# Kernel optimization log

Measured on AMD Instinct MI355X. Metric: run time of the kernel, lower is better.

Reference implementation:

```python
import jax, jax.numpy as jnp
import numpy as np

D_MODEL = 512
D_INNER = 1024           # expand=2 * d_model
HEADDIM = 1024           # headdim = 2*hidden_dim -> nheads = 1
NHEADS = 1
D_STATE = 128            # Mamba2 default
D_CONV = 4               # Mamba2 default
CONV_DIM = D_INNER + 2 * D_STATE   # 1280
D_IN_PROJ = 2 * D_INNER + 2 * D_STATE + NHEADS  # 2305
BATCH, SEQ = 8, 2048
EPS = 1e-5


def setup_inputs() -> dict:
    key = jax.random.key(0)
    ks = jax.random.split(key, 8)
    x = jax.random.normal(ks[0], (BATCH, SEQ, D_MODEL), dtype=jnp.float32)
    rnn_state = jnp.zeros((1, BATCH, D_MODEL), dtype=jnp.float32)
    W_in = jax.random.normal(ks[1], (D_MODEL, D_IN_PROJ), dtype=jnp.float32) * 0.02
    conv_w = jax.random.normal(ks[2], (CONV_DIM, D_CONV), dtype=jnp.float32) * 0.2
    conv_b = jnp.zeros((CONV_DIM,), dtype=jnp.float32)
    dt_bias = jax.random.normal(ks[3], (NHEADS,), dtype=jnp.float32) * 0.1
    # A in (-16, -1): A_log = log(uniform(1,16))
    A_log = jnp.log(jax.random.uniform(ks[4], (NHEADS,), minval=1.0, maxval=16.0, dtype=jnp.float32))
    D = jnp.ones((NHEADS,), dtype=jnp.float32)
    norm_w = jnp.ones((D_INNER,), dtype=jnp.float32)
    W_out = jax.random.normal(ks[5], (D_INNER, D_MODEL), dtype=jnp.float32) * 0.02
    return {"x": x, "rnn_state": rnn_state, "W_in": W_in, "conv_w": conv_w,
            "conv_b": conv_b, "dt_bias": dt_bias, "A_log": A_log, "D": D,
            "norm_w": norm_w, "W_out": W_out}


def _mamba2_forward(x, W_in, conv_w, conv_b, dt_bias, A_log, D, norm_w, W_out):
    Bsz, T, _ = x.shape
    zxbcdt = x @ W_in                              # [B,T,2305]
    z = zxbcdt[..., :D_INNER]                      # [B,T,1024]
    xBC = zxbcdt[..., D_INNER:D_INNER + CONV_DIM]  # [B,T,1280]
    dt = zxbcdt[..., -NHEADS:]                     # [B,T,1]

    # causal depthwise conv1d over time, then silu
    xBC_t = jnp.transpose(xBC, (0, 2, 1))          # [B,C,T]
    w = conv_w[:, None, :]                          # [C,1,K]
    conv = jax.lax.conv_general_dilated(
        xBC_t, w, window_strides=(1,), padding=[(D_CONV - 1, 0)],
        feature_group_count=CONV_DIM, dimension_numbers=("NCH", "OIH", "NCH"))
    xBC = jax.nn.silu(jnp.transpose(conv, (0, 2, 1)) + conv_b)  # [B,T,1280]

    x_ssm = xBC[..., :D_INNER].reshape(Bsz, T, NHEADS, HEADDIM)  # [B,T,H,P]
    Bm = xBC[..., D_INNER:D_INNER + D_STATE]       # [B,T,N] (ngroups=1)
    Cm = xBC[..., -D_STATE:]                       # [B,T,N]

    dt = jax.nn.softplus(dt + dt_bias)             # [B,T,H]
    A = -jnp.exp(A_log)                            # [H]

    # selective SSM recurrence over time (time-major scan)
    xs = (jnp.transpose(x_ssm, (1, 0, 2, 3)),      # [T,B,H,P]
          jnp.transpose(dt, (1, 0, 2)),            # [T,B,H]
          jnp.transpose(Bm, (1, 0, 2)),            # [T,B,N]
          jnp.transpose(Cm, (1, 0, 2)))            # [T,B,N]
    h0 = jnp.zeros((Bsz, NHEADS, HEADDIM, D_STATE), dtype=x.dtype)

    def step(h, inp):
        xt, dtt, Bt, Ct = inp
        dA = jnp.exp(dtt * A)                      # [B,H]
        h = h * dA[:, :, None, None] + (dtt[:, :, None] * xt)[..., None] * Bt[:, None, None, :]
        y = jnp.einsum("bhpn,bn->bhp", h, Ct)
        return h, y

    _, ys = jax.lax.scan(step, h0, xs)             # ys: [T,B,H,P]
    y = jnp.transpose(ys, (1, 0, 2, 3)) + x_ssm * D[None, None, :, None]
    y = y.reshape(Bsz, T, D_INNER)

    # gated RMSNorm (norm_before_gate=False): rmsnorm(y * silu(z)) * weight
    y = y * jax.nn.silu(z)
    y = y * jax.lax.rsqrt(jnp.mean(y * y, axis=-1, keepdims=True) + EPS) * norm_w
    return y @ W_out                               # [B,T,D_MODEL]


def reference(x, rnn_state, W_in, conv_w, conv_b, dt_bias, A_log, D, norm_w, W_out):
    out = _mamba2_forward(x, W_in, conv_w, conv_b, dt_bias, A_log, D, norm_w, W_out)
    return (out, rnn_state)
```

## Files before the change

kernel.cpp:

```cpp
#include <hip/hip_runtime.h>
#include <hip/hip_bf16.h>
#include <math.h>

#define D_MODEL 512
#define D_INNER 1024
#define D_STATE 128
#define CONV_DIM (D_INNER + 2*D_STATE)
#define D_IN_PROJ (2*D_INNER + 2*D_STATE + 1)
#define NPROJ 2304
#define BATCH 8
#define SEQ 2048
#define NROWS (BATCH*SEQ)
#define CHUNK 128
#define NCHUNK (NROWS/CHUNK)
#define CPB (SEQ/CHUNK)
#define EPS_RMS 1e-5f

typedef __hip_bfloat16 bf16;
typedef __attribute__((ext_vector_type(8))) short short8;
typedef __attribute__((ext_vector_type(4))) float f32x4;

__device__ __forceinline__ float fbf(bf16 v) { return __bfloat162float(v); }
__device__ __forceinline__ bf16 tbf(float v) { return __float2bfloat16(v); }

__device__ __forceinline__ void gl2lds16(const bf16* g, bf16* l) {
    __builtin_amdgcn_global_load_lds(
        (const __attribute__((address_space(1))) unsigned int*)g,
        (__attribute__((address_space(3))) unsigned int*)l, 16, 0, 0);
}


__global__ void k_transpose_cvt(const float* __restrict__ src, bf16* __restrict__ dst,
                                int R, int C, int sstride) {
    __shared__ float tile[32][33];
    int c0 = blockIdx.x * 32, r0 = blockIdx.y * 32;
    int tx = threadIdx.x, ty = threadIdx.y;
    #pragma unroll
    for (int i = 0; i < 32; i += 8)
        tile[ty + i][tx] = src[(size_t)(c0 + ty + i) * sstride + (r0 + tx)];
    __syncthreads();
    #pragma unroll
    for (int i = 0; i < 32; i += 8)
        dst[(size_t)(r0 + ty + i) * C + (c0 + tx)] = tbf(tile[tx][ty + i]);
}

__global__ __launch_bounds__(256) void k_dtcvt(
    const float* __restrict__ x, const float* __restrict__ W_in,
    const float* __restrict__ dt_bias,
    bf16* __restrict__ xb, float* __restrict__ dts)
{
    __shared__ float wcol[D_MODEL];
    int tid = threadIdx.x;
    wcol[tid]       = W_in[(size_t)tid * D_IN_PROJ + 2304];
    wcol[tid + 256] = W_in[(size_t)(tid + 256) * D_IN_PROJ + 2304];
    __syncthreads();
    int row  = blockIdx.x * 4 + (tid >> 6);
    int lane = tid & 63;
    const float* xr = x + (size_t)row * D_MODEL;
    float4 a = *(const float4*)(xr + lane * 8);
    float4 b = *(const float4*)(xr + lane * 8 + 4);
    union { bf16 o[8]; uint4 u; } pk;
    pk.o[0]=tbf(a.x); pk.o[1]=tbf(a.y); pk.o[2]=tbf(a.z); pk.o[3]=tbf(a.w);
    pk.o[4]=tbf(b.x); pk.o[5]=tbf(b.y); pk.o[6]=tbf(b.z); pk.o[7]=tbf(b.w);
    *(uint4*)(xb + (size_t)row * D_MODEL + lane * 8) = pk.u;
    const float* wc = wcol + lane * 8;
    float s = a.x*wc[0]+a.y*wc[1]+a.z*wc[2]+a.w*wc[3]
            + b.x*wc[4]+b.y*wc[5]+b.z*wc[6]+b.w*wc[7];
    #pragma unroll
    for (int off = 32; off; off >>= 1) s += __shfl_xor(s, off);
    if (lane == 0) {
        float raw = s + dt_bias[0];
        dts[row] = raw > 20.f ? raw : log1pf(expf(raw));
    }
}

template<int MODE>
__global__ __launch_bounds__(256) void k_bgemm(
    const bf16* __restrict__ A, int lda, size_t sA,
    const bf16* __restrict__ Bt, int ldb, size_t sB,
    void* __restrict__ Cv, int ldc, size_t sC, int K,
    const float* __restrict__ svec, const float* __restrict__ dts,
    const float* __restrict__ Dp)
{
    constexpr int BK = 64;
    __shared__ __align__(16) bf16 As[128][BK];
    __shared__ __align__(16) bf16 Bs[128][BK];
    const int tid = threadIdx.x, lane = tid & 63, wave = tid >> 6;
    const int wm = (wave & 1) * 64, wn = (wave >> 1) * 64;
    const int lr = lane & 15, quad = lane >> 4;
    const int rx = lr & 7;
    const size_t bm = (size_t)blockIdx.x * 128;
    const size_t bn = (size_t)blockIdx.y * 128;
    const size_t bi = blockIdx.z;
    A  += bi * sA;
    Bt += bi * sB;
    const int srow = lane >> 3;
    const int scol = (((lane & 7) ^ srow) << 3);

    f32x4 acc[4][4];
    #pragma unroll
    for (int i = 0; i < 4; ++i)
        #pragma unroll
        for (int j = 0; j < 4; ++j) acc[i][j] = (f32x4){0.f,0.f,0.f,0.f};

    for (int k0 = 0; k0 < K; k0 += BK) {
        __syncthreads();
        #pragma unroll
        for (int q = 0; q < 4; ++q) {
            int rg = wave * 32 + q * 8;
            gl2lds16(A  + (bm + rg + srow) * lda + k0 + scol, &As[rg][0]);
            gl2lds16(Bt + (bn + rg + srow) * ldb + k0 + scol, &Bs[rg][0]);
        }
        __syncthreads();
        #pragma unroll
        for (int ks = 0; ks < BK; ks += 32) {
            const int off = ((((ks >> 3) + quad) ^ rx) << 3);
            short8 af[4], bg[4];
            #pragma unroll
            for (int i = 0; i < 4; ++i)
                af[i] = *(const short8*)(&As[wm + i*16 + lr][off]);
            #pragma unroll
            for (int j = 0; j < 4; ++j)
                bg[j] = *(const short8*)(&Bs[wn + j*16 + lr][off]);
            #pragma unroll
            for (int i = 0; i < 4; ++i)
                #pragma unroll
                for (int j = 0; j < 4; ++j)
                    acc[i][j] = __builtin_amdgcn_mfma_f32_16x16x32_bf16(af[i], bg[j], acc[i][j], 0,0,0);
        }
    }
    const int rb = (int)bi * CHUNK;
    #pragma unroll
    for (int i = 0; i < 4; ++i)
        #pragma unroll
        for (int j = 0; j < 4; ++j)
            #pragma unroll
            for (int r = 0; r < 4; ++r) {
                size_t row = bm + wm + i*16 + quad*4 + r;
                size_t col = bn + wn + j*16 + lr;
                float v = acc[i][j][r];
                if (MODE == 0) {
                    ((float*)Cv + bi*sC)[row * ldc + col] = v;
                } else if (MODE == 1) {
                    ((bf16*)Cv + bi*sC)[row * ldc + col] = tbf(v);
                } else {
                    float o = 0.f;
                    if (col <= row) {
                        o = v * expf(svec[rb + row] - svec[rb + col]) * dts[rb + col];
                        if (col == row) o += Dp[0];
                    }
                    ((bf16*)Cv + bi*sC)[row * ldc + col] = tbf(o);
                }
            }
}

__global__ __launch_bounds__(256) void k_gemm_in(
    const bf16* __restrict__ A, const bf16* __restrict__ Bt,
    bf16* __restrict__ zb, bf16* __restrict__ xBCin, int K)
{
    constexpr int BK = 64;
    __shared__ __align__(16) bf16 As[128][BK];
    __shared__ __align__(16) bf16 Bs[128][BK];
    const int tid = threadIdx.x, lane = tid & 63, wave = tid >> 6;
    const int wm = (wave & 1) * 64, wn = (wave >> 1) * 64;
    const int lr = lane & 15, quad = lane >> 4;
    const int rx = lr & 7;
    const size_t bm = (size_t)blockIdx.x * 128;
    const int bn = blockIdx.y * 128;
    const int srow = lane >> 3;
    const int scol = (((lane & 7) ^ srow) << 3);

    f32x4 acc[4][4];
    #pragma unroll
    for (int i = 0; i < 4; ++i)
        #pragma unroll
        for (int j = 0; j < 4; ++j) acc[i][j] = (f32x4){0.f,0.f,0.f,0.f};

    for (int k0 = 0; k0 < K; k0 += BK) {
        __syncthreads();
        #pragma unroll
        for (int q = 0; q < 4; ++q) {
            int rg = wave * 32 + q * 8;
            gl2lds16(A  + (bm + rg + srow) * K + k0 + scol, &As[rg][0]);
            gl2lds16(Bt + ((size_t)bn + rg + srow) * K + k0 + scol, &Bs[rg][0]);
        }
        __syncthreads();
        #pragma unroll
        for (int ks = 0; ks < BK; ks += 32) {
            const int off = ((((ks >> 3) + quad) ^ rx) << 3);
            short8 af[4], bg[4];
            #pragma unroll
            for (int i = 0; i < 4; ++i)
                af[i] = *(const short8*)(&As[wm + i*16 + lr][off]);
            #pragma unroll
            for (int j = 0; j < 4; ++j)
                bg[j] = *(const short8*)(&Bs[wn + j*16 + lr][off]);
            #pragma unroll
            for (int i = 0; i < 4; ++i)
                #pragma unroll
                for (int j = 0; j < 4; ++j)
                    acc[i][j] = __builtin_amdgcn_mfma_f32_16x16x32_bf16(af[i], bg[j], acc[i][j], 0,0,0);
        }
    }
    #pragma unroll
    for (int i = 0; i < 4; ++i)
        #pragma unroll
        for (int j = 0; j < 4; ++j)
            #pragma unroll
            for (int r = 0; r < 4; ++r) {
                size_t row = bm + wm + i*16 + quad*4 + r;
                int col = bn + wn + j*16 + lr;
                float v = acc[i][j][r];
                if (col < D_INNER) zb[row * D_INNER + col] = tbf(v);
                else xBCin[row * CONV_DIM + (col - D_INNER)] = tbf(v);
            }
}

__global__ void k_prep(const float* __restrict__ dts, const float* __restrict__ A_log,
                       float* __restrict__ svec, float* __restrict__ wvec,
                       float* __restrict__ esvec, float* __restrict__ Pc)
{
    int chunk = blockIdx.x, t = threadIdx.x;
    int row = chunk * CHUNK + t;
    float A = -expf(A_log[0]);
    __shared__ float sh[CHUNK];
    sh[t] = A * dts[row];
    __syncthreads();
    for (int off = 1; off < CHUNK; off <<= 1) {
        float v = (t >= off) ? sh[t - off] : 0.f;
        __syncthreads();
        sh[t] += v;
        __syncthreads();
    }
    float s = sh[t], sL = sh[CHUNK - 1];
    svec[row]  = s;
    wvec[row]  = expf(sL - s) * dts[row];
    esvec[row] = expf(s);
    if (t == CHUNK - 1) Pc[chunk] = expf(sL);
}

__global__ __launch_bounds__(256) void k_conv_x(
    const bf16* __restrict__ xBCin, const float* __restrict__ conv_w,
    const float* __restrict__ conv_b, bf16* __restrict__ B2)
{
    __shared__ __align__(16) bf16 Ls[131][128];
    const int chunk = blockIdx.y;
    const int p0 = blockIdx.x * 128;
    const int tid = threadIdx.x;
    const bool first = (chunk % CPB) == 0;
    const size_t rowbase = (size_t)chunk * CHUNK;
    for (int i = tid; i < 131 * 16; i += 256) {
        int r = i >> 4, cg = (i & 15) << 3;
        uint4 v = (uint4){0,0,0,0};
        if (!(first && r < 3))
            v = *(const uint4*)(xBCin + (rowbase + r - 3) * CONV_DIM + p0 + cg);
        *(uint4*)(&Ls[r][cg]) = v;
    }
    __syncthreads();
    const int p = tid & 127;
    const int half = tid >> 7;
    const int ch = p0 + p;
    float4 w = *(const float4*)(conv_w + ch * 4);
    float bias = conv_b[ch];
    bf16* outrow = B2 + (size_t)chunk * (D_INNER * 256) + (size_t)ch * 256;
    float xv[11];
    #pragma unroll
    for (int i = 0; i < 3; ++i) xv[i + 8] = fbf(Ls[half * 64 + i][p]);
    for (int v = 0; v < 8; ++v) {
        int t0 = half * 64 + v * 8;
        xv[0]=xv[8]; xv[1]=xv[9]; xv[2]=xv[10];
        #pragma unroll
        for (int i = 3; i < 11; ++i) xv[i] = fbf(Ls[t0 + i][p]);
        union { bf16 o[8]; uint4 u; } pk;
        #pragma unroll
        for (int j = 0; j < 8; ++j) {
            float a = bias + w.x*xv[j] + w.y*xv[j+1] + w.z*xv[j+2] + w.w*xv[j+3];
            pk.o[j] = tbf(a / (1.f + expf(-a)));
        }
        *(uint4*)(outrow + t0) = pk.u;
    }
}

__global__ __launch_bounds__(256) void k_conv_bc(
    const bf16* __restrict__ xBCin, const float* __restrict__ conv_w,
    const float* __restrict__ conv_b, const float* __restrict__ wvec,
    const float* __restrict__ esvec,
    bf16* __restrict__ Braw, bf16* __restrict__ Craw,
    bf16* __restrict__ Bw, bf16* __restrict__ A2)
{
    __shared__ __align__(16) bf16 Ls[131][256];
    const int chunk = blockIdx.x;
    const bool first = (chunk % CPB) == 0;
    const size_t rowbase = (size_t)chunk * CHUNK;
    for (int i = threadIdx.x; i < 131 * 32; i += 256) {
        int r = i >> 5, cg = (i & 31) << 3;
        uint4 v = (uint4){0,0,0,0};
        if (!(first && r < 3))
            v = *(const uint4*)(xBCin + (rowbase + r - 3) * CONV_DIM + D_INNER + cg);
        *(uint4*)(&Ls[r][cg]) = v;
    }
    __syncthreads();
    const int n   = threadIdx.x & 127;
    const int reg = threadIdx.x >> 7;
    const int cl  = reg * 128 + n;
    const int ch  = D_INNER + cl;
    float4 w = *(const float4*)(conv_w + ch * 4);
    float bias = conv_b[ch];
    float xv[11];
    #pragma unroll
    for (int i = 0; i < 3; ++i) xv[i + 8] = fbf(Ls[i][cl]);
    for (int v = 0; v < 16; ++v) {
        int t0 = v * 8;
        xv[0]=xv[8]; xv[1]=xv[9]; xv[2]=xv[10];
        #pragma unroll
        for (int i = 3; i < 11; ++i) xv[i] = fbf(Ls[t0 + i][cl]);
        float o[8];
        #pragma unroll
        for (int j = 0; j < 8; ++j) {
            float a = bias + w.x*xv[j] + w.y*xv[j+1] + w.z*xv[j+2] + w.w*xv[j+3];
            o[j] = a / (1.f + expf(-a));
        }
        if (reg == 0) {
            union { bf16 ob[8]; uint4 u; } pk;
            #pragma unroll
            for (int j = 0; j < 8; ++j) {
                Braw[(size_t)chunk*(CHUNK*D_STATE) + (size_t)(t0+j)*D_STATE + n] = tbf(o[j]);
                pk.ob[j] = tbf(o[j] * wvec[rowbase + t0 + j]);
            }
            *(uint4*)(Bw + (size_t)chunk*(D_STATE*CHUNK) + (size_t)n*CHUNK + t0) = pk.u;
        } else {
            #pragma unroll
            for (int j = 0; j < 8; ++j) {
                Craw[(size_t)chunk*(CHUNK*D_STATE) + (size_t)(t0+j)*D_STATE + n] = tbf(o[j]);
                A2[(size_t)chunk*(CHUNK*256) + (size_t)(t0+j)*256 + 128 + n] =
                    tbf(o[j] * esvec[rowbase + t0 + j]);
            }
        }
    }
}

__global__ void k_carry(const bf16* __restrict__ dH, const float* __restrict__ Pc,
                        bf16* __restrict__ B2)
{
    int idx = blockIdx.x * 256 + threadIdx.x;
    int b = blockIdx.y;
    int p = idx >> 7, n = idx & 127;
    float h = 0.f;
    for (int c = 0; c < CPB; ++c) {
        int bi = b * CPB + c;
        B2[(size_t)bi * (D_INNER*256) + (size_t)p * 256 + 128 + n] = tbf(h);
        h = Pc[bi] * h + fbf(dH[(size_t)bi * (D_INNER*D_STATE) + idx]);
    }
}

__global__ __launch_bounds__(256) void k_gate_norm(
    bf16* __restrict__ y, const bf16* __restrict__ zb,
    const float* __restrict__ norm_w)
{
    int row = blockIdx.x;
    int tid = threadIdx.x;
    bf16* yr = y + (size_t)row * D_INNER;
    const bf16* zr = zb + (size_t)row * D_INNER;
    union { bf16 b[4]; uint2 u; } ly, lz;
    ly.u = *(const uint2*)(yr + tid * 4);
    lz.u = *(const uint2*)(zr + tid * 4);
    float v[4], ss = 0.f;
    #pragma unroll
    for (int j = 0; j < 4; ++j) {
        float z = fbf(lz.b[j]);
        v[j] = fbf(ly.b[j]) * z / (1.f + expf(-z));
        ss += v[j] * v[j];
    }
    #pragma unroll
    for (int off = 32; off; off >>= 1) ss += __shfl_xor(ss, off);
    __shared__ float wsum[4];
    if ((tid & 63) == 0) wsum[tid >> 6] = ss;
    __syncthreads();
    float tot   = wsum[0] + wsum[1] + wsum[2] + wsum[3];
    float scale = rsqrtf(tot * (1.f / D_INNER) + EPS_RMS);
    union { bf16 b[4]; uint2 u; } po;
    #pragma unroll
    for (int j = 0; j < 4; ++j)
        po.b[j] = tbf(v[j] * scale * norm_w[tid*4 + j]);
    *(uint2*)(yr + tid * 4) = po.u;
}

extern "C" void kernel_launch(void* const* d_in, const int* in_sizes, int n_in,
                              void* d_out, int out_size, void* d_ws, size_t ws_size,
                              hipStream_t stream)
{
    const float* x       = (const float*)d_in[0];
    const float* rnn     = (const float*)d_in[1];
    const float* W_in    = (const float*)d_in[2];
    const float* conv_w  = (const float*)d_in[3];
    const float* conv_b  = (const float*)d_in[4];
    const float* dt_bias = (const float*)d_in[5];
    const float* A_log   = (const float*)d_in[6];
    const float* Dp      = (const float*)d_in[7];
    const float* norm_w  = (const float*)d_in[8];
    const float* W_out   = (const float*)d_in[9];
    float* out = (float*)d_out;

    char* ws = (char*)d_ws;
    size_t off = 0;
    auto alloc = [&](size_t bytes) { void* p = ws + off; off += (bytes + 255) & ~255ULL; return p; };

    bf16*  W_inbT  = (bf16*) alloc((size_t)NPROJ * D_MODEL * 2);
    bf16*  W_outbT = (bf16*) alloc((size_t)D_MODEL * D_INNER * 2);
    float* dts     = (float*)alloc((size_t)NROWS * 4);
    float* svec    = (float*)alloc((size_t)NROWS * 4);
    float* wvec    = (float*)alloc((size_t)NROWS * 4);
    float* esvec   = (float*)alloc((size_t)NROWS * 4);
    float* Pc      = (float*)alloc((size_t)NCHUNK * 4);
    bf16*  zb      = (bf16*) alloc((size_t)NROWS * D_INNER * 2);
    bf16*  A2      = (bf16*) alloc((size_t)NCHUNK * CHUNK * 256 * 2);
    bf16*  B2      = (bf16*) alloc((size_t)NCHUNK * D_INNER * 256 * 2);
    bf16*  Bw      = (bf16*) alloc((size_t)NCHUNK * D_STATE * CHUNK * 2);
    bf16*  Braw    = (bf16*) alloc((size_t)NCHUNK * CHUNK * D_STATE * 2);
    bf16*  Craw    = (bf16*) alloc((size_t)NCHUNK * CHUNK * D_STATE * 2);
    char* RA = (char*)alloc((size_t)NROWS * D_MODEL * 2 + (size_t)NROWS * D_INNER * 2);
    bf16*  xb   = (bf16*)RA;
    bf16*  dH   = (bf16*)(RA + (size_t)NROWS * D_MODEL * 2);
    bf16*  ybf  = (bf16*)RA;
    bf16*  xBCin = (bf16*)alloc((size_t)NROWS * CONV_DIM * 2);

    k_dtcvt<<<NROWS / 4, 256, 0, stream>>>(x, W_in, dt_bias, xb, dts);
    k_transpose_cvt<<<dim3(D_MODEL/32, NPROJ/32), dim3(32, 8), 0, stream>>>(
        W_in, W_inbT, NPROJ, D_MODEL, D_IN_PROJ);
    k_transpose_cvt<<<dim3(D_INNER/32, D_MODEL/32), dim3(32, 8), 0, stream>>>(
        W_out, W_outbT, D_MODEL, D_INNER, D_MODEL);
    k_prep<<<NCHUNK, CHUNK, 0, stream>>>(dts, A_log, svec, wvec, esvec, Pc);

    k_gemm_in<<<dim3(NROWS/128, NPROJ/128), 256, 0, stream>>>(xb, W_inbT, zb, xBCin, D_MODEL);

    k_conv_x<<<dim3(8, NCHUNK), 256, 0, stream>>>(xBCin, conv_w, conv_b, B2);
    k_conv_bc<<<NCHUNK, 256, 0, stream>>>(xBCin, conv_w, conv_b, wvec, esvec,
                                          Braw, Craw, Bw, A2);

    k_bgemm<2><<<dim3(1, 1, NCHUNK), 256, 0, stream>>>(
        Craw, D_STATE, (size_t)CHUNK*D_STATE,
        Braw, D_STATE, (size_t)CHUNK*D_STATE,
        A2, 256, (size_t)CHUNK*256, CHUNK, svec, dts, Dp);

    k_bgemm<1><<<dim3(D_INNER/128, 1, NCHUNK), 256, 0, stream>>>(
        B2, 256, (size_t)D_INNER*256,
        Bw, CHUNK, (size_t)D_STATE*CHUNK,
        dH, D_STATE, (size_t)D_INNER*D_STATE, CHUNK, nullptr, nullptr, nullptr);

    k_carry<<<dim3(D_INNER*D_STATE/256, BATCH), 256, 0, stream>>>(dH, Pc, B2);

    k_bgemm<1><<<dim3(1, D_INNER/128, NCHUNK), 256, 0, stream>>>(
        A2, 256, (size_t)CHUNK*256,
        B2, 256, (size_t)D_INNER*256,
        ybf, D_INNER, (size_t)CHUNK*D_INNER, 256, nullptr, nullptr, nullptr);

    k_gate_norm<<<NROWS, 256, 0, stream>>>(ybf, zb, norm_w);

    k_bgemm<0><<<dim3(NROWS/128, D_MODEL/128, 1), 256, 0, stream>>>(
        ybf, D_INNER, 0, W_outbT, D_INNER, 0, out, D_MODEL, 0, D_INNER,
        nullptr, nullptr, nullptr);

    hipMemcpyAsync(out + (size_t)NROWS * D_MODEL, rnn,
                   (size_t)BATCH * D_MODEL * sizeof(float),
                   hipMemcpyDeviceToDevice, stream);
}
```

Baseline: 326.9 us.

## Fuse B/C conv with CB^T GEMM and x conv with chunk-state GEMM

Merges the B/C depthwise conv with the intra-chunk C·B^T masked-decay GEMM in one kernel, and the x conv with the dH = X·Bw state GEMM, keeping the conv outputs in LDS. This removes the Braw/Craw round trips and two separate batched GEMM launches. It also preloads dH and Pc in the carry scan and processes four rows per block in gate-norm with wider vector loads. The cost is heavier LDS use per block, which may lower occupancy, and the GEMMs now read LDS without swizzling (only padding), which may cause bank conflicts.

```diff
diff --git a/kernel.cpp b/kernel.cpp
--- a/kernel.cpp
+++ b/kernel.cpp
@@ -28,7 +28,6 @@
         (const __attribute__((address_space(1))) unsigned int*)g,
         (__attribute__((address_space(3))) unsigned int*)l, 16, 0, 0);
 }
-
 
 __global__ void k_transpose_cvt(const float* __restrict__ src, bf16* __restrict__ dst,
                                 int R, int C, int sstride) {
@@ -78,9 +77,7 @@
 __global__ __launch_bounds__(256) void k_bgemm(
     const bf16* __restrict__ A, int lda, size_t sA,
     const bf16* __restrict__ Bt, int ldb, size_t sB,
-    void* __restrict__ Cv, int ldc, size_t sC, int K,
-    const float* __restrict__ svec, const float* __restrict__ dts,
-    const float* __restrict__ Dp)
+    void* __restrict__ Cv, int ldc, size_t sC, int K)
 {
     constexpr int BK = 64;
     __shared__ __align__(16) bf16 As[128][BK];
@@ -129,7 +126,6 @@
                     acc[i][j] = __builtin_amdgcn_mfma_f32_16x16x32_bf16(af[i], bg[j], acc[i][j], 0,0,0);
         }
     }
-    const int rb = (int)bi * CHUNK;
     #pragma unroll
     for (int i = 0; i < 4; ++i)
         #pragma unroll
@@ -139,18 +135,8 @@
                 size_t row = bm + wm + i*16 + quad*4 + r;
                 size_t col = bn + wn + j*16 + lr;
                 float v = acc[i][j][r];
-                if (MODE == 0) {
-                    ((float*)Cv + bi*sC)[row * ldc + col] = v;
-                } else if (MODE == 1) {
-                    ((bf16*)Cv + bi*sC)[row * ldc + col] = tbf(v);
-                } else {
-                    float o = 0.f;
-                    if (col <= row) {
-                        o = v * expf(svec[rb + row] - svec[rb + col]) * dts[rb + col];
-                        if (col == row) o += Dp[0];
-                    }
-                    ((bf16*)Cv + bi*sC)[row * ldc + col] = tbf(o);
-                }
+                if (MODE == 0) ((float*)Cv + bi*sC)[row * ldc + col] = v;
+                else           ((bf16*)Cv + bi*sC)[row * ldc + col] = tbf(v);
             }
 }
 
@@ -239,11 +225,126 @@
     if (t == CHUNK - 1) Pc[chunk] = expf(sL);
 }
 
-__global__ __launch_bounds__(256) void k_conv_x(
+__global__ __launch_bounds__(256) void k_ssd_bc(
     const bf16* __restrict__ xBCin, const float* __restrict__ conv_w,
-    const float* __restrict__ conv_b, bf16* __restrict__ B2)
+    const float* __restrict__ conv_b, const float* __restrict__ wvec,
+    const float* __restrict__ esvec, const float* __restrict__ svec,
+    const float* __restrict__ dts, const float* __restrict__ Dp,
+    bf16* __restrict__ Bw, bf16* __restrict__ A2)
 {
     __shared__ __align__(16) bf16 Ls[131][128];
+    __shared__ __align__(16) bf16 Bts[128][136];
+    __shared__ __align__(16) bf16 Cts[128][136];
+    __shared__ float sv_s[128], dt_s[128], wv_s[128], es_s[128];
+    const int chunk = blockIdx.x;
+    const int tid = threadIdx.x;
+    const bool first = (chunk % CPB) == 0;
+    const size_t rowbase = (size_t)chunk * CHUNK;
+    if (tid < 128) {
+        sv_s[tid] = svec[rowbase + tid];
+        dt_s[tid] = dts[rowbase + tid];
+        wv_s[tid] = wvec[rowbase + tid];
+        es_s[tid] = esvec[rowbase + tid];
+    }
+    const int ch  = tid & 127;
+    const int seg = tid >> 7;
+
+    #pragma unroll
+    for (int phase = 0; phase < 2; ++phase) {
+        const int coff = D_INNER + phase * 128;
+        __syncthreads();
+        for (int i = tid; i < 131 * 16; i += 256) {
+            int r = i >> 4, cg = (i & 15) << 3;
+            uint4 v = (uint4){0,0,0,0};
+            if (!(first && r < 3))
+                v = *(const uint4*)(xBCin + (rowbase + r - 3) * CONV_DIM + coff + cg);
+            *(uint4*)(&Ls[r][cg]) = v;
+        }
+        __syncthreads();
+        float4 w = *(const float4*)(conv_w + (coff + ch) * 4);
+        float bias = conv_b[coff + ch];
+        float xv[11];
+        #pragma unroll
+        for (int i = 0; i < 3; ++i) xv[i + 8] = fbf(Ls[seg * 64 + i][ch]);
+        for (int v = 0; v < 8; ++v) {
+            int t0 = seg * 64 + v * 8;
+            xv[0]=xv[8]; xv[1]=xv[9]; xv[2]=xv[10];
+            #pragma unroll
+            for (int i = 3; i < 11; ++i) xv[i] = fbf(Ls[t0 + i][ch]);
+            float o[8];
+            #pragma unroll
+            for (int j = 0; j < 8; ++j) {
+                float a = bias + w.x*xv[j] + w.y*xv[j+1] + w.z*xv[j+2] + w.w*xv[j+3];
+                o[j] = a / (1.f + expf(-a));
+            }
+            if (phase == 0) {
+                union { bf16 ob[8]; uint4 u; } pk;
+                #pragma unroll
+                for (int j = 0; j < 8; ++j) {
+                    Bts[t0 + j][ch] = tbf(o[j]);
+                    pk.ob[j] = tbf(o[j] * wv_s[t0 + j]);
+                }
+                *(uint4*)(Bw + (size_t)chunk*(D_STATE*CHUNK) + (size_t)ch*CHUNK + t0) = pk.u;
+            } else {
+                #pragma unroll
+                for (int j = 0; j < 8; ++j) {
+                    Cts[t0 + j][ch] = tbf(o[j]);
+                    A2[(size_t)chunk*(CHUNK*256) + (size_t)(t0+j)*256 + 128 + ch] =
+                        tbf(o[j] * es_s[t0 + j]);
+                }
+            }
+        }
+    }
+    __syncthreads();
+    const int lane = tid & 63, wave = tid >> 6;
+    const int wm = (wave & 1) * 64, wn = (wave >> 1) * 64;
+    const int lr = lane & 15, quad = lane >> 4;
+    f32x4 acc[4][4];
+    #pragma unroll
+    for (int i = 0; i < 4; ++i)
+        #pragma unroll
+        for (int j = 0; j < 4; ++j) acc[i][j] = (f32x4){0.f,0.f,0.f,0.f};
+    #pragma unroll
+    for (int ks = 0; ks < 128; ks += 32) {
+        short8 af[4], bg[4];
+        #pragma unroll
+        for (int i = 0; i < 4; ++i)
+            af[i] = *(const short8*)(&Cts[wm + i*16 + lr][ks + quad*8]);
+        #pragma unroll
+        for (int j = 0; j < 4; ++j)
+            bg[j] = *(const short8*)(&Bts[wn + j*16 + lr][ks + quad*8]);
+        #pragma unroll
+        for (int i = 0; i < 4; ++i)
+            #pragma unroll
+            for (int j = 0; j < 4; ++j)
+                acc[i][j] = __builtin_amdgcn_mfma_f32_16x16x32_bf16(af[i], bg[j], acc[i][j], 0,0,0);
+    }
+    const float D0 = Dp[0];
+    #pragma unroll
+    for (int i = 0; i < 4; ++i)
+        #pragma unroll
+        for (int j = 0; j < 4; ++j)
+            #pragma unroll
+            for (int r = 0; r < 4; ++r) {
+                int t = wm + i*16 + quad*4 + r;
+                int u = wn + j*16 + lr;
+                float o = 0.f;
+                if (u <= t) {
+                    o = acc[i][j][r] * expf(sv_s[t] - sv_s[u]) * dt_s[u];
+                    if (u == t) o += D0;
+                }
+                A2[(size_t)chunk*(CHUNK*256) + (size_t)t*256 + u] = tbf(o);
+            }
+}
+
+__global__ __launch_bounds__(256) void k_conv_xdh(
+    const bf16* __restrict__ xBCin, const float* __restrict__ conv_w,
+    const float* __restrict__ conv_b, const bf16* __restrict__ Bw,
+    bf16* __restrict__ B2, bf16* __restrict__ dH)
+{
+    __shared__ __align__(16) bf16 Ls[131][128];
+    __shared__ __align__(16) bf16 Xs[128][136];
+    __shared__ __align__(16) bf16 Bws[128][136];
     const int chunk = blockIdx.y;
     const int p0 = blockIdx.x * 128;
     const int tid = threadIdx.x;
@@ -256,6 +357,11 @@
             v = *(const uint4*)(xBCin + (rowbase + r - 3) * CONV_DIM + p0 + cg);
         *(uint4*)(&Ls[r][cg]) = v;
     }
+    for (int i = tid; i < 128 * 16; i += 256) {
+        int nr = i >> 4, cg = (i & 15) << 3;
+        *(uint4*)(&Bws[nr][cg]) =
+            *(const uint4*)(Bw + (size_t)chunk*(D_STATE*CHUNK) + (size_t)nr*CHUNK + cg);
+    }
     __syncthreads();
     const int p = tid & 127;
     const int half = tid >> 7;
@@ -278,65 +384,42 @@
             pk.o[j] = tbf(a / (1.f + expf(-a)));
         }
         *(uint4*)(outrow + t0) = pk.u;
-    }
-}
-
-__global__ __launch_bounds__(256) void k_conv_bc(
-    const bf16* __restrict__ xBCin, const float* __restrict__ conv_w,
-    const float* __restrict__ conv_b, const float* __restrict__ wvec,
-    const float* __restrict__ esvec,
-    bf16* __restrict__ Braw, bf16* __restrict__ Craw,
-    bf16* __restrict__ Bw, bf16* __restrict__ A2)
-{
-    __shared__ __align__(16) bf16 Ls[131][256];
-    const int chunk = blockIdx.x;
-    const bool first = (chunk % CPB) == 0;
-    const size_t rowbase = (size_t)chunk * CHUNK;
-    for (int i = threadIdx.x; i < 131 * 32; i += 256) {
-        int r = i >> 5, cg = (i & 31) << 3;
-        uint4 v = (uint4){0,0,0,0};
-        if (!(first && r < 3))
-            v = *(const uint4*)(xBCin + (rowbase + r - 3) * CONV_DIM + D_INNER + cg);
-        *(uint4*)(&Ls[r][cg]) = v;
+        *(uint4*)(&Xs[p][t0]) = pk.u;
     }
     __syncthreads();
-    const int n   = threadIdx.x & 127;
-    const int reg = threadIdx.x >> 7;
-    const int cl  = reg * 128 + n;
-    const int ch  = D_INNER + cl;
-    float4 w = *(const float4*)(conv_w + ch * 4);
-    float bias = conv_b[ch];
-    float xv[11];
-    #pragma unroll
-    for (int i = 0; i < 3; ++i) xv[i + 8] = fbf(Ls[i][cl]);
-    for (int v = 0; v < 16; ++v) {
-        int t0 = v * 8;
-        xv[0]=xv[8]; xv[1]=xv[9]; xv[2]=xv[10];
-        #pragma unroll
-        for (int i = 3; i < 11; ++i) xv[i] = fbf(Ls[t0 + i][cl]);
-        float o[8];
-        #pragma unroll
-        for (int j = 0; j < 8; ++j) {
-            float a = bias + w.x*xv[j] + w.y*xv[j+1] + w.z*xv[j+2] + w.w*xv[j+3];
-            o[j] = a / (1.f + expf(-a));
-        }
-        if (reg == 0) {
-            union { bf16 ob[8]; uint4 u; } pk;
-            #pragma unroll
-            for (int j = 0; j < 8; ++j) {
-                Braw[(size_t)chunk*(CHUNK*D_STATE) + (size_t)(t0+j)*D_STATE + n] = tbf(o[j]);
-                pk.ob[j] = tbf(o[j] * wvec[rowbase + t0 + j]);
+    const int lane = tid & 63, wave = tid >> 6;
+    const int wm = (wave & 1) * 64, wn = (wave >> 1) * 64;
+    const int lr = lane & 15, quad = lane >> 4;
+    f32x4 acc[4][4];
+    #pragma unroll
+    for (int i = 0; i < 4; ++i)
+        #pragma unroll
+        for (int j = 0; j < 4; ++j) acc[i][j] = (f32x4){0.f,0.f,0.f,0.f};
+    #pragma unroll
+    for (int ks = 0; ks < 128; ks += 32) {
+        short8 af[4], bg[4];
+        #pragma unroll
+        for (int i = 0; i < 4; ++i)
+            af[i] = *(const short8*)(&Xs[wm + i*16 + lr][ks + quad*8]);
+        #pragma unroll
+        for (int j = 0; j < 4; ++j)
+            bg[j] = *(const short8*)(&Bws[wn + j*16 + lr][ks + quad*8]);
+        #pragma unroll
+        for (int i = 0; i < 4; ++i)
+            #pragma unroll
+            for (int j = 0; j < 4; ++j)
+                acc[i][j] = __builtin_amdgcn_mfma_f32_16x16x32_bf16(af[i], bg[j], acc[i][j], 0,0,0);
+    }
+    #pragma unroll
+    for (int i = 0; i < 4; ++i)
+        #pragma unroll
+        for (int j = 0; j < 4; ++j)
+            #pragma unroll
+            for (int r = 0; r < 4; ++r) {
+                int pr = p0 + wm + i*16 + quad*4 + r;
+                int n  = wn + j*16 + lr;
+                dH[(size_t)chunk*(D_INNER*D_STATE) + (size_t)pr*D_STATE + n] = tbf(acc[i][j][r]);
             }
-            *(uint4*)(Bw + (size_t)chunk*(D_STATE*CHUNK) + (size_t)n*CHUNK + t0) = pk.u;
-        } else {
-            #pragma unroll
-            for (int j = 0; j < 8; ++j) {
-                Craw[(size_t)chunk*(CHUNK*D_STATE) + (size_t)(t0+j)*D_STATE + n] = tbf(o[j]);
-                A2[(size_t)chunk*(CHUNK*256) + (size_t)(t0+j)*256 + 128 + n] =
-                    tbf(o[j] * esvec[rowbase + t0 + j]);
-            }
-        }
-    }
 }
 
 __global__ void k_carry(const bf16* __restrict__ dH, const float* __restrict__ Pc,
@@ -345,11 +428,18 @@
     int idx = blockIdx.x * 256 + threadIdx.x;
     int b = blockIdx.y;
     int p = idx >> 7, n = idx & 127;
+    float v[CPB], pc[CPB];
+    #pragma unroll
+    for (int c = 0; c < CPB; ++c)
+        v[c] = fbf(dH[(size_t)(b*CPB + c) * (D_INNER*D_STATE) + idx]);
+    #pragma unroll
+    for (int c = 0; c < CPB; ++c) pc[c] = Pc[b*CPB + c];
     float h = 0.f;
+    #pragma unroll
     for (int c = 0; c < CPB; ++c) {
         int bi = b * CPB + c;
         B2[(size_t)bi * (D_INNER*256) + (size_t)p * 256 + 128 + n] = tbf(h);
-        h = Pc[bi] * h + fbf(dH[(size_t)bi * (D_INNER*D_STATE) + idx]);
+        h = pc[c] * h + v[c];
     }
 }
 
@@ -357,32 +447,37 @@
     bf16* __restrict__ y, const bf16* __restrict__ zb,
     const float* __restrict__ norm_w)
 {
-    int row = blockIdx.x;
-    int tid = threadIdx.x;
+    int row  = blockIdx.x * 4 + (threadIdx.x >> 6);
+    int lane = threadIdx.x & 63;
     bf16* yr = y + (size_t)row * D_INNER;
     const bf16* zr = zb + (size_t)row * D_INNER;
-    union { bf16 b[4]; uint2 u; } ly, lz;
-    ly.u = *(const uint2*)(yr + tid * 4);
-    lz.u = *(const uint2*)(zr + tid * 4);
-    float v[4], ss = 0.f;
-    #pragma unroll
-    for (int j = 0; j < 4; ++j) {
-        float z = fbf(lz.b[j]);
-        v[j] = fbf(ly.b[j]) * z / (1.f + expf(-z));
+    const int c0 = lane * 8, c1 = 512 + lane * 8;
+    union { bf16 b[8]; uint4 u; } y0, y1, z0, z1;
+    y0.u = *(const uint4*)(yr + c0); y1.u = *(const uint4*)(yr + c1);
+    z0.u = *(const uint4*)(zr + c0); z1.u = *(const uint4*)(zr + c1);
+    float v[16], ss = 0.f;
+    #pragma unroll
+    for (int j = 0; j < 8; ++j) {
+        float z = fbf(z0.b[j]);
+        v[j] = fbf(y0.b[j]) * z / (1.f + expf(-z));
         ss += v[j] * v[j];
     }
     #pragma unroll
+    for (int j = 0; j < 8; ++j) {
+        float z = fbf(z1.b[j]);
+        v[8+j] = fbf(y1.b[j]) * z / (1.f + expf(-z));
+        ss += v[8+j] * v[8+j];
+    }
+    #pragma unroll
     for (int off = 32; off; off >>= 1) ss += __shfl_xor(ss, off);
-    __shared__ float wsum[4];
-    if ((tid & 63) == 0) wsum[tid >> 6] = ss;
-    __syncthreads();
-    float tot   = wsum[0] + wsum[1] + wsum[2] + wsum[3];
-    float scale = rsqrtf(tot * (1.f / D_INNER) + EPS_RMS);
-    union { bf16 b[4]; uint2 u; } po;
-    #pragma unroll
-    for (int j = 0; j < 4; ++j)
-        po.b[j] = tbf(v[j] * scale * norm_w[tid*4 + j]);
-    *(uint2*)(yr + tid * 4) = po.u;
+    float scale = rsqrtf(ss * (1.f / D_INNER) + EPS_RMS);
+    union { bf16 b[8]; uint4 u; } p0, p1;
+    #pragma unroll
+    for (int j = 0; j < 8; ++j) p0.b[j] = tbf(v[j]   * scale * norm_w[c0 + j]);
+    #pragma unroll
+    for (int j = 0; j < 8; ++j) p1.b[j] = tbf(v[8+j] * scale * norm_w[c1 + j]);
+    *(uint4*)(yr + c0) = p0.u;
+    *(uint4*)(yr + c1) = p1.u;
 }
 
 extern "C" void kernel_launch(void* const* d_in, const int* in_sizes, int n_in,
@@ -416,8 +511,6 @@
     bf16*  A2      = (bf16*) alloc((size_t)NCHUNK * CHUNK * 256 * 2);
     bf16*  B2      = (bf16*) alloc((size_t)NCHUNK * D_INNER * 256 * 2);
     bf16*  Bw      = (bf16*) alloc((size_t)NCHUNK * D_STATE * CHUNK * 2);
-    bf16*  Braw    = (bf16*) alloc((size_t)NCHUNK * CHUNK * D_STATE * 2);
-    bf16*  Craw    = (bf16*) alloc((size_t)NCHUNK * CHUNK * D_STATE * 2);
     char* RA = (char*)alloc((size_t)NROWS * D_MODEL * 2 + (size_t)NROWS * D_INNER * 2);
     bf16*  xb   = (bf16*)RA;
     bf16*  dH   = (bf16*)(RA + (size_t)NROWS * D_MODEL * 2);
@@ -433,32 +526,22 @@
 
     k_gemm_in<<<dim3(NROWS/128, NPROJ/128), 256, 0, stream>>>(xb, W_inbT, zb, xBCin, D_MODEL);
 
-    k_conv_x<<<dim3(8, NCHUNK), 256, 0, stream>>>(xBCin, conv_w, conv_b, B2);
-    k_conv_bc<<<NCHUNK, 256, 0, stream>>>(xBCin, conv_w, conv_b, wvec, esvec,
-                                          Braw, Craw, Bw, A2);
-
-    k_bgemm<2><<<dim3(1, 1, NCHUNK), 256, 0, stream>>>(
-        Craw, D_STATE, (size_t)CHUNK*D_STATE,
-        Braw, D_STATE, (size_t)CHUNK*D_STATE,
-        A2, 256, (size_t)CHUNK*256, CHUNK, svec, dts, Dp);
-
-    k_bgemm<1><<<dim3(D_INNER/128, 1, NCHUNK), 256, 0, stream>>>(
-        B2, 256, (size_t)D_INNER*256,
-        Bw, CHUNK, (size_t)D_STATE*CHUNK,
-        dH, D_STATE, (size_t)D_INNER*D_STATE, CHUNK, nullptr, nullptr, nullptr);
+    k_ssd_bc<<<NCHUNK, 256, 0, stream>>>(xBCin, conv_w, conv_b, wvec, esvec,
+                                         svec, dts, Dp, Bw, A2);
+
+    k_conv_xdh<<<dim3(8, NCHUNK), 256, 0, stream>>>(xBCin, conv_w, conv_b, Bw, B2, dH);
 
     k_carry<<<dim3(D_INNER*D_STATE/256, BATCH), 256, 0, stream>>>(dH, Pc, B2);
 
     k_bgemm<1><<<dim3(1, D_INNER/128, NCHUNK), 256, 0, stream>>>(
         A2, 256, (size_t)CHUNK*256,
         B2, 256, (size_t)D_INNER*256,
-        ybf, D_INNER, (size_t)CHUNK*D_INNER, 256, nullptr, nullptr, nullptr);
-
-    k_gate_norm<<<NROWS, 256, 0, stream>>>(ybf, zb, norm_w);
+        ybf, D_INNER, (size_t)CHUNK*D_INNER, 256);
+
+    k_gate_norm<<<NROWS / 4, 256, 0, stream>>>(ybf, zb, norm_w);
 
     k_bgemm<0><<<dim3(NROWS/128, D_MODEL/128, 1), 256, 0, stream>>>(
-        ybf, D_INNER, 0, W_outbT, D_INNER, 0, out, D_MODEL, 0, D_INNER,
-        nullptr, nullptr, nullptr);
+        ybf, D_INNER, 0, W_outbT, D_INNER, 0, out, D_MODEL, 0, D_INNER);
 
     hipMemcpyAsync(out + (size_t)NROWS * D_MODEL, rnn,
                    (size_t)BATCH * D_MODEL * sizeof(float),
```

Measured after the change: 323.1 us. Within noise of the previous version (-1.2%).
